# Kernel tuning notes

Measured on AMD Instinct MI355X. Metric: run time of the kernel, lower is better.

## Reference

```python
import jax, jax.numpy as jnp
import numpy as np

N_HEADS = 16
N_KV_HEADS = 8
DIM = 2048
HEAD_DIM = DIM // N_HEADS  # 128
N_REP = N_HEADS // N_KV_HEADS


def _rope(t, cos, sin):
    # t: [B, S, H, D]; cos/sin: [S, D//2]
    t2 = t.reshape(*t.shape[:-1], -1, 2)  # [B,S,H,D/2,2]
    p1, p2 = t2[..., 0], t2[..., 1]
    c = cos[None, :, None, :]
    s = sin[None, :, None, :]
    r1 = p1 * c - p2 * s
    r2 = p1 * s + p2 * c
    return jnp.stack((r1, r2), axis=-1).reshape(t.shape)


def setup_inputs() -> dict:
    key = jax.random.key(0)
    ks = jax.random.split(key, 7)
    B, S = 2, 2048
    x = jax.random.normal(ks[0], (B, S, DIM), dtype=jnp.float32)
    freqs_cos = jax.random.normal(ks[1], (S, HEAD_DIM // 2), dtype=jnp.float32)
    freqs_sin = jax.random.normal(ks[2], (S, HEAD_DIM // 2), dtype=jnp.float32)
    sc = 1.0 / np.sqrt(DIM)
    wq = jax.random.normal(ks[3], (DIM, N_HEADS * HEAD_DIM), dtype=jnp.float32) * sc
    wk = jax.random.normal(ks[4], (DIM, N_KV_HEADS * HEAD_DIM), dtype=jnp.float32) * sc
    wv = jax.random.normal(ks[5], (DIM, N_KV_HEADS * HEAD_DIM), dtype=jnp.float32) * sc
    wo = jax.random.normal(ks[6], (N_HEADS * HEAD_DIM, DIM), dtype=jnp.float32) * sc
    return {"x": x, "freqs_cos": freqs_cos, "freqs_sin": freqs_sin,
            "wq": wq, "wk": wk, "wv": wv, "wo": wo}


def reference(x, freqs_cos, freqs_sin, wq, wk, wv, wo):
    B, S, _ = x.shape
    xq = (x @ wq).reshape(B, S, N_HEADS, HEAD_DIM)
    xk = (x @ wk).reshape(B, S, N_KV_HEADS, HEAD_DIM)
    xv = (x @ wv).reshape(B, S, N_KV_HEADS, HEAD_DIM)
    xq = _rope(xq, freqs_cos, freqs_sin)
    xk = _rope(xk, freqs_cos, freqs_sin)
    # GQA repeat_kv: [B,S,Hkv,D] -> [B,S,Hkv*n_rep,D]
    xk = jnp.repeat(xk, N_REP, axis=2)
    xv = jnp.repeat(xv, N_REP, axis=2)
    q = xq.transpose(0, 2, 1, 3)  # [B,H,S,D]
    k = xk.transpose(0, 2, 1, 3)
    v = xv.transpose(0, 2, 1, 3)
    scale = 1.0 / np.sqrt(HEAD_DIM)
    scores = jnp.einsum('bhqd,bhkd->bhqk', q, k) * scale
    causal = jnp.tril(jnp.ones((S, S), dtype=bool))
    scores = jnp.where(causal[None, None], scores, -jnp.inf)
    probs = jax.nn.softmax(scores.astype(jnp.float32), axis=-1).astype(q.dtype)
    out = jnp.einsum('bhqk,bhkd->bhqd', probs, v)
    out = out.transpose(0, 2, 1, 3).reshape(B, S, N_HEADS * HEAD_DIM)
    return out @ wo
```

## Files before the change

### kernel.cpp

```cpp
#include <hip/hip_runtime.h>
#include <cstdint>
#include <cstddef>

#define S_LEN 2048
#define DIM_   2048
#define NH   16
#define NKV  8
#define HD   128

typedef __attribute__((ext_vector_type(8))) __bf16 bf16x8;
typedef __attribute__((ext_vector_type(4))) float  f32x4;

typedef const __attribute__((address_space(1))) void* gptr_t;
typedef __attribute__((address_space(3))) void*       sptr_t;

static __device__ __forceinline__ float bf2f(unsigned short u) {
  union { unsigned int i; float f; } v; v.i = ((unsigned int)u) << 16; return v.f;
}
static __device__ __forceinline__ unsigned short f2bf(float f) {
  union { float f; unsigned int i; } v; v.f = f;
  unsigned int u = v.i;
  unsigned int r = (u + 0x7FFFu + ((u >> 16) & 1u)) >> 16;
  return (unsigned short)r;
}

#define QSCALE 0.12751744f

__global__ void k_prep(const float* __restrict__ x, unsigned short* __restrict__ xb,
                       const float* __restrict__ wq, const float* __restrict__ wk,
                       const float* __restrict__ wv, const float* __restrict__ wo,
                       unsigned short* __restrict__ wqkvT, unsigned short* __restrict__ woT) {
  int bid = blockIdx.x;
  if (bid < 8192) {
    int i = bid * 256 + threadIdx.x;
    float4 v = ((const float4*)x)[i];
    ushort4 o; o.x = f2bf(v.x); o.y = f2bf(v.y); o.z = f2bf(v.z); o.w = f2bf(v.w);
    ((ushort4*)xb)[i] = o;
    return;
  }
  bid -= 8192;
  const float* src; unsigned short* dst; int N, ntx;
  if (bid < 4096)      { src = wq; dst = wqkvT;                       N = 2048; ntx = 64; }
  else if (bid < 6144) { bid -= 4096; src = wk; dst = wqkvT + (size_t)2048 * 2048; N = 1024; ntx = 32; }
  else if (bid < 8192) { bid -= 6144; src = wv; dst = wqkvT + (size_t)3072 * 2048; N = 1024; ntx = 32; }
  else                 { bid -= 8192; src = wo; dst = woT;            N = 2048; ntx = 64; }
  const int K = 2048;
  __shared__ float tile[32][33];
  int lx = threadIdx.x & 31, ly = threadIdx.x >> 5;
  int r0 = (bid / ntx) * 32, c0 = (bid % ntx) * 32;
  #pragma unroll
  for (int r = 0; r < 32; r += 8)
    tile[ly + r][lx] = src[(size_t)(r0 + ly + r) * N + c0 + lx];
  __syncthreads();
  #pragma unroll
  for (int r = 0; r < 32; r += 8)
    dst[(size_t)(c0 + ly + r) * K + r0 + lx] = f2bf(tile[lx][ly + r]);
}

template<int MODE>
__global__ __launch_bounds__(256, 2) void k_gemm_bt(
    const unsigned short* __restrict__ A, const unsigned short* __restrict__ BT,
    void* __restrict__ C, int N, int K,
    const float* __restrict__ fc, const float* __restrict__ fs,
    unsigned short* __restrict__ kb, unsigned short* __restrict__ vb) {
  __shared__ __align__(16) unsigned short Asm[128 * 64];
  __shared__ __align__(16) unsigned short Bsm[128 * 64];
  const int t = threadIdx.x;
  const int lane = t & 63, w = t >> 6;
  const int wm = (w >> 1) * 64, wn = (w & 1) * 64;
  const int col = lane & 15, quad = lane >> 4;
  const int m0 = blockIdx.y * 128, n0 = blockIdx.x * 128;

  f32x4 acc[4][4];
  #pragma unroll
  for (int i = 0; i < 4; i++)
    #pragma unroll
    for (int j = 0; j < 4; j++) acc[i][j] = (f32x4){0.f, 0.f, 0.f, 0.f};

  for (int kk = 0; kk < K; kk += 64) {
    #pragma unroll
    for (int r = 0; r < 4; ++r) {
      int c = t + r * 256;
      int c0 = (t & ~63) + r * 256;
      int row = c >> 3;
      int kcs = (c & 7) ^ (row & 7);
      const unsigned short* gA = A + (size_t)(m0 + row) * K + kk + kcs * 8;
      const unsigned short* gB = BT + (size_t)(n0 + row) * K + kk + kcs * 8;
      __builtin_amdgcn_global_load_lds((gptr_t)gA, (sptr_t)(&Asm[c0 * 8]), 16, 0, 0);
      __builtin_amdgcn_global_load_lds((gptr_t)gB, (sptr_t)(&Bsm[c0 * 8]), 16, 0, 0);
    }
    __syncthreads();
    #pragma unroll
    for (int kc2 = 0; kc2 < 2; kc2++) {
      bf16x8 af[4], bf[4];
      #pragma unroll
      for (int mi = 0; mi < 4; mi++) {
        int rowA = wm + mi * 16 + col;
        af[mi] = *(const bf16x8*)(&Asm[rowA * 64 + (((kc2 * 4 + quad) ^ (col & 7)) * 8)]);
      }
      #pragma unroll
      for (int ni = 0; ni < 4; ni++) {
        int rowB = wn + ni * 16 + col;
        bf[ni] = *(const bf16x8*)(&Bsm[rowB * 64 + (((kc2 * 4 + quad) ^ (col & 7)) * 8)]);
      }
      #pragma unroll
      for (int mi = 0; mi < 4; mi++)
        #pragma unroll
        for (int ni = 0; ni < 4; ni++)
          acc[mi][ni] = __builtin_amdgcn_mfma_f32_16x16x32_bf16(af[mi], bf[ni], acc[mi][ni], 0, 0, 0);
    }
    __syncthreads();
  }

  #pragma unroll
  for (int mi = 0; mi < 4; mi++) {
    int row_base = m0 + wm + mi * 16 + quad * 4;
    #pragma unroll
    for (int ni = 0; ni < 4; ni++) {
      int col_g = n0 + wn + ni * 16 + col;
      if (MODE == 1) {
        float* O = (float*)C;
        #pragma unroll
        for (int r = 0; r < 4; r++) O[(size_t)(row_base + r) * N + col_g] = acc[mi][ni][r];
      } else {
        int region = col_g >> 10;
        if (region < 3) {
          int ri = (col_g & 127) >> 1;
          float sgn = (col_g & 1) ? 1.f : -1.f;
          unsigned short* qO = (unsigned short*)C;
          #pragma unroll
          for (int r = 0; r < 4; r++) {
            int row = row_base + r;
            int s = row & (S_LEN - 1);
            float cv = fc[s * 64 + ri], sv = fs[s * 64 + ri];
            float val = acc[mi][ni][r];
            float other = __shfl_xor(val, 1);
            float res = val * cv + sgn * other * sv;
            if (region < 2) qO[(size_t)row * 2048 + col_g] = f2bf(res * QSCALE);
            else            kb[(size_t)row * 1024 + (col_g - 2048)] = f2bf(res);
          }
        } else {
          int n_local = col_g - 3072;
          int b = row_base >> 11, s = row_base & (S_LEN - 1);
          int kvh = n_local >> 7, d = n_local & (HD - 1);
          ushort4 o4;
          o4.x = f2bf(acc[mi][ni][0]); o4.y = f2bf(acc[mi][ni][1]);
          o4.z = f2bf(acc[mi][ni][2]); o4.w = f2bf(acc[mi][ni][3]);
          *(ushort4*)(&vb[((size_t)((b * NKV + kvh) * HD + d)) * S_LEN + s]) = o4;
        }
      }
    }
  }
}

#define KLD 136
#define VLD 72
__global__ __launch_bounds__(1024) void k_attn(
    const unsigned short* __restrict__ q, const unsigned short* __restrict__ k,
    const unsigned short* __restrict__ vT, unsigned short* __restrict__ ao) {
  __shared__ __align__(16) unsigned short Ksm[64 * KLD];
  __shared__ __align__(16) unsigned short Vsm[128 * VLD];
  __shared__ __align__(16) unsigned short Psm[16 * 16 * VLD];
  const int t = threadIdx.x;
  const int lane = t & 63, w = t >> 6;
  const int col = lane & 15, quad = lane >> 4;
  const int g = blockIdx.x;
  const int b = g >> 3, kvh = g & 7;
  const int h = kvh * 2 + ((w >> 2) & 1);
  const int y = blockIdx.y;
  const int my_qt = (w < 8) ? y : (31 - y);
  const int qrow = my_qt * 64 + (w & 3) * 16;
  unsigned short* Pw = &Psm[w * 16 * VLD];

  bf16x8 qf[4];
  const size_t qbase = ((size_t)(b * S_LEN) + qrow + col) * DIM_ + h * HD;
  #pragma unroll
  for (int kc = 0; kc < 4; kc++) qf[kc] = *(const bf16x8*)(q + qbase + kc * 32 + quad * 8);

  f32x4 o[8];
  #pragma unroll
  for (int i = 0; i < 8; i++) o[i] = (f32x4){0.f, 0.f, 0.f, 0.f};
  float m_i[4] = {-1e30f, -1e30f, -1e30f, -1e30f};
  float l_i[4] = {0.f, 0.f, 0.f, 0.f};

  const int nkt = 32 - y;
  for (int kt = 0; kt < nkt; ++kt) {
    { int i = t >> 4, dc = t & 15;
      *(uint4*)(&Ksm[i * KLD + dc * 8]) =
          *(const uint4*)(k + ((size_t)(b * S_LEN + kt * 64 + i)) * (NKV * HD) + kvh * HD + dc * 8);
      int d = t >> 3, kc2 = t & 7;
      *(uint4*)(&Vsm[d * VLD + kc2 * 8]) =
          *(const uint4*)(vT + ((size_t)((b * NKV + kvh) * HD + d)) * S_LEN + kt * 64 + kc2 * 8);
    }
    __syncthreads();

    if (kt <= my_qt) {
      float p[4][4];
      #pragma unroll
      for (int nt = 0; nt < 4; nt++) {
        f32x4 s_acc = (f32x4){0.f, 0.f, 0.f, 0.f};
        #pragma unroll
        for (int kc = 0; kc < 4; kc++) {
          bf16x8 kf = *(const bf16x8*)(&Ksm[(nt * 16 + col) * KLD + kc * 32 + quad * 8]);
          s_acc = __builtin_amdgcn_mfma_f32_16x16x32_bf16(qf[kc], kf, s_acc, 0, 0, 0);
        }
        #pragma unroll
        for (int r = 0; r < 4; r++) p[nt][r] = s_acc[r];
      }
      if (kt == my_qt) {
        #pragma unroll
        for (int nt = 0; nt < 4; nt++) {
          int key = kt * 64 + nt * 16 + col;
          #pragma unroll
          for (int r = 0; r < 4; r++) {
            int rg = qrow + quad * 4 + r;
            if (key > rg) p[nt][r] = -1e30f;
          }
        }
      }
      float mnew[4], alpha[4];
      #pragma unroll
      for (int r = 0; r < 4; r++) {
        float mx = fmaxf(fmaxf(p[0][r], p[1][r]), fmaxf(p[2][r], p[3][r]));
        mx = fmaxf(mx, __shfl_xor(mx, 1));
        mx = fmaxf(mx, __shfl_xor(mx, 2));
        mx = fmaxf(mx, __shfl_xor(mx, 4));
        mx = fmaxf(mx, __shfl_xor(mx, 8));
        mnew[r] = fmaxf(m_i[r], mx);
        alpha[r] = exp2f(m_i[r] - mnew[r]);
        m_i[r] = mnew[r];
      }
      float rsum[4] = {0.f, 0.f, 0.f, 0.f};
      #pragma unroll
      for (int nt = 0; nt < 4; nt++)
        #pragma unroll
        for (int r = 0; r < 4; r++) {
          float e = exp2f(p[nt][r] - mnew[r]);
          p[nt][r] = e;
          rsum[r] += e;
        }
      #pragma unroll
      for (int r = 0; r < 4; r++) {
        float rs = rsum[r];
        rs += __shfl_xor(rs, 1);
        rs += __shfl_xor(rs, 2);
        rs += __shfl_xor(rs, 4);
        rs += __shfl_xor(rs, 8);
        l_i[r] = l_i[r] * alpha[r] + rs;
      }
      #pragma unroll
      for (int dt = 0; dt < 8; dt++)
        #pragma unroll
        for (int r = 0; r < 4; r++) o[dt][r] *= alpha[r];

      #pragma unroll
      for (int nt = 0; nt < 4; nt++)
        #pragma unroll
        for (int r = 0; r < 4; r++)
          Pw[(quad * 4 + r) * VLD + nt * 16 + col] = f2bf(p[nt][r]);
      asm volatile("s_waitcnt lgkmcnt(0)" ::: "memory");
      bf16x8 pf[2];
      #pragma unroll
      for (int kc2 = 0; kc2 < 2; kc2++)
        pf[kc2] = *(const bf16x8*)(&Pw[col * VLD + kc2 * 32 + quad * 8]);

      #pragma unroll
      for (int dt = 0; dt < 8; dt++) {
        #pragma unroll
        for (int kc2 = 0; kc2 < 2; kc2++) {
          bf16x8 vf = *(const bf16x8*)(&Vsm[(dt * 16 + col) * VLD + kc2 * 32 + quad * 8]);
          o[dt] = __builtin_amdgcn_mfma_f32_16x16x32_bf16(pf[kc2], vf, o[dt], 0, 0, 0);
        }
      }
    }
    __syncthreads();
  }

  #pragma unroll
  for (int dt = 0; dt < 8; dt++) {
    int dcol = h * HD + dt * 16 + col;
    #pragma unroll
    for (int r = 0; r < 4; r++) {
      int rg = qrow + quad * 4 + r;
      ao[((size_t)(b * S_LEN) + rg) * DIM_ + dcol] = f2bf(o[dt][r] / l_i[r]);
    }
  }
}

extern "C" void kernel_launch(void* const* d_in, const int* in_sizes, int n_in,
                              void* d_out, int out_size, void* d_ws, size_t ws_size,
                              hipStream_t stream) {
  const float* x  = (const float*)d_in[0];
  const float* fc = (const float*)d_in[1];
  const float* fs = (const float*)d_in[2];
  const float* wq = (const float*)d_in[3];
  const float* wk = (const float*)d_in[4];
  const float* wv = (const float*)d_in[5];
  const float* wo = (const float*)d_in[6];
  float* out = (float*)d_out;

  char* ws = (char*)d_ws;
  const size_t MB = 1024 * 1024;
  unsigned short* xb    = (unsigned short*)(ws + 0 * MB);
  unsigned short* wqkvT = (unsigned short*)(ws + 16 * MB);
  unsigned short* woT   = (unsigned short*)(ws + 32 * MB);
  unsigned short* qb    = (unsigned short*)(ws + 40 * MB);
  unsigned short* kb    = (unsigned short*)(ws + 56 * MB);
  unsigned short* vT    = (unsigned short*)(ws + 64 * MB);
  unsigned short* ao    = (unsigned short*)(ws + 72 * MB);

  k_prep<<<dim3(20480), dim3(256), 0, stream>>>(x, xb, wq, wk, wv, wo, wqkvT, woT);
  k_gemm_bt<3><<<dim3(32, 32), dim3(256), 0, stream>>>(xb, wqkvT, (void*)qb, 4096, 2048, fc, fs, kb, vT);
  k_attn<<<dim3(16, 16), dim3(1024), 0, stream>>>(qb, kb, vT, ao);
  k_gemm_bt<1><<<dim3(16, 32), dim3(256), 0, stream>>>(ao, woT, (void*)out, 2048, 2048, nullptr, nullptr, nullptr, nullptr);
}
```

Measured before the change: 357.6 us.

## Transpose attention MFMA operands to keep P in registers and drop LDS staging

Swaps MFMA operand order so each lane holds a full query row's scores (query on the column index), so row max and sum need only two cross-quad shuffles and each lane keeps scalar m/l. The P tile is rebuilt for the PV MFMA by packing bf16 pairs and exchanging them through lane shuffles rather than a round trip through LDS, which also removes the Psm shared buffer. The output is now written as ushort4 vectors, and launch bounds add a min-blocks hint. The cost is many more shuffle instructions and selects per tile.

```diff
diff --git a/kernel.cpp b/kernel.cpp
--- a/kernel.cpp
+++ b/kernel.cpp
@@ -22,6 +22,9 @@
   unsigned int u = v.i;
   unsigned int r = (u + 0x7FFFu + ((u >> 16) & 1u)) >> 16;
   return (unsigned short)r;
+}
+static __device__ __forceinline__ unsigned int pack2bf(float lo, float hi) {
+  return ((unsigned int)f2bf(hi) << 16) | (unsigned int)f2bf(lo);
 }
 
 #define QSCALE 0.12751744f
@@ -155,12 +158,11 @@
 
 #define KLD 136
 #define VLD 72
-__global__ __launch_bounds__(1024) void k_attn(
+__global__ __launch_bounds__(1024, 4) void k_attn(
     const unsigned short* __restrict__ q, const unsigned short* __restrict__ k,
     const unsigned short* __restrict__ vT, unsigned short* __restrict__ ao) {
   __shared__ __align__(16) unsigned short Ksm[64 * KLD];
   __shared__ __align__(16) unsigned short Vsm[128 * VLD];
-  __shared__ __align__(16) unsigned short Psm[16 * 16 * VLD];
   const int t = threadIdx.x;
   const int lane = t & 63, w = t >> 6;
   const int col = lane & 15, quad = lane >> 4;
@@ -170,18 +172,21 @@
   const int y = blockIdx.y;
   const int my_qt = (w < 8) ? y : (31 - y);
   const int qrow = my_qt * 64 + (w & 3) * 16;
-  unsigned short* Pw = &Psm[w * 16 * VLD];
+  const int qg = qrow + col;
 
   bf16x8 qf[4];
-  const size_t qbase = ((size_t)(b * S_LEN) + qrow + col) * DIM_ + h * HD;
+  const size_t qbase = ((size_t)(b * S_LEN) + qg) * DIM_ + h * HD;
   #pragma unroll
   for (int kc = 0; kc < 4; kc++) qf[kc] = *(const bf16x8*)(q + qbase + kc * 32 + quad * 8);
 
   f32x4 o[8];
   #pragma unroll
   for (int i = 0; i < 8; i++) o[i] = (f32x4){0.f, 0.f, 0.f, 0.f};
-  float m_i[4] = {-1e30f, -1e30f, -1e30f, -1e30f};
-  float l_i[4] = {0.f, 0.f, 0.f, 0.f};
+  float m_i = -1e30f, l_i = 0.f;
+
+  const int ls0 = ((quad & 1) * 2) * 16 + col;
+  const int ls1 = ls0 + 16;
+  const bool hi_nt = (quad >> 1) != 0;
 
   const int nkt = 32 - y;
   for (int kt = 0; kt < nkt; ++kt) {
@@ -202,7 +207,7 @@
         #pragma unroll
         for (int kc = 0; kc < 4; kc++) {
           bf16x8 kf = *(const bf16x8*)(&Ksm[(nt * 16 + col) * KLD + kc * 32 + quad * 8]);
-          s_acc = __builtin_amdgcn_mfma_f32_16x16x32_bf16(qf[kc], kf, s_acc, 0, 0, 0);
+          s_acc = __builtin_amdgcn_mfma_f32_16x16x32_bf16(kf, qf[kc], s_acc, 0, 0, 0);
         }
         #pragma unroll
         for (int r = 0; r < 4; r++) p[nt][r] = s_acc[r];
@@ -210,80 +215,77 @@
       if (kt == my_qt) {
         #pragma unroll
         for (int nt = 0; nt < 4; nt++) {
-          int key = kt * 64 + nt * 16 + col;
+          int key = kt * 64 + nt * 16 + quad * 4;
           #pragma unroll
-          for (int r = 0; r < 4; r++) {
-            int rg = qrow + quad * 4 + r;
-            if (key > rg) p[nt][r] = -1e30f;
-          }
-        }
-      }
-      float mnew[4], alpha[4];
-      #pragma unroll
-      for (int r = 0; r < 4; r++) {
-        float mx = fmaxf(fmaxf(p[0][r], p[1][r]), fmaxf(p[2][r], p[3][r]));
-        mx = fmaxf(mx, __shfl_xor(mx, 1));
-        mx = fmaxf(mx, __shfl_xor(mx, 2));
-        mx = fmaxf(mx, __shfl_xor(mx, 4));
-        mx = fmaxf(mx, __shfl_xor(mx, 8));
-        mnew[r] = fmaxf(m_i[r], mx);
-        alpha[r] = exp2f(m_i[r] - mnew[r]);
-        m_i[r] = mnew[r];
-      }
-      float rsum[4] = {0.f, 0.f, 0.f, 0.f};
+          for (int r = 0; r < 4; r++)
+            if (key + r > qg) p[nt][r] = -1e30f;
+        }
+      }
+      float mx = p[0][0];
       #pragma unroll
       for (int nt = 0; nt < 4; nt++)
         #pragma unroll
+        for (int r = 0; r < 4; r++) mx = fmaxf(mx, p[nt][r]);
+      mx = fmaxf(mx, __shfl_xor(mx, 16));
+      mx = fmaxf(mx, __shfl_xor(mx, 32));
+      float mnew = fmaxf(m_i, mx);
+      float alpha = exp2f(m_i - mnew);
+      m_i = mnew;
+      float rs = 0.f;
+      #pragma unroll
+      for (int nt = 0; nt < 4; nt++)
+        #pragma unroll
         for (int r = 0; r < 4; r++) {
-          float e = exp2f(p[nt][r] - mnew[r]);
+          float e = exp2f(p[nt][r] - mnew);
           p[nt][r] = e;
-          rsum[r] += e;
-        }
-      #pragma unroll
-      for (int r = 0; r < 4; r++) {
-        float rs = rsum[r];
-        rs += __shfl_xor(rs, 1);
-        rs += __shfl_xor(rs, 2);
-        rs += __shfl_xor(rs, 4);
-        rs += __shfl_xor(rs, 8);
-        l_i[r] = l_i[r] * alpha[r] + rs;
-      }
+          rs += e;
+        }
+      rs += __shfl_xor(rs, 16);
+      rs += __shfl_xor(rs, 32);
+      l_i = l_i * alpha + rs;
       #pragma unroll
       for (int dt = 0; dt < 8; dt++)
         #pragma unroll
-        for (int r = 0; r < 4; r++) o[dt][r] *= alpha[r];
-
-      #pragma unroll
-      for (int nt = 0; nt < 4; nt++)
-        #pragma unroll
-        for (int r = 0; r < 4; r++)
-          Pw[(quad * 4 + r) * VLD + nt * 16 + col] = f2bf(p[nt][r]);
-      asm volatile("s_waitcnt lgkmcnt(0)" ::: "memory");
-      bf16x8 pf[2];
-      #pragma unroll
-      for (int kc2 = 0; kc2 < 2; kc2++)
-        pf[kc2] = *(const bf16x8*)(&Pw[col * VLD + kc2 * 32 + quad * 8]);
-
-      #pragma unroll
-      for (int dt = 0; dt < 8; dt++) {
-        #pragma unroll
-        for (int kc2 = 0; kc2 < 2; kc2++) {
+        for (int r = 0; r < 4; r++) o[dt][r] *= alpha;
+
+      unsigned int pk[4][2];
+      #pragma unroll
+      for (int nt = 0; nt < 4; nt++) {
+        pk[nt][0] = pack2bf(p[nt][0], p[nt][1]);
+        pk[nt][1] = pack2bf(p[nt][2], p[nt][3]);
+      }
+      #pragma unroll
+      for (int kc2 = 0; kc2 < 2; kc2++) {
+        union { bf16x8 v; unsigned int d[4]; } pf;
+        unsigned int a0 = (unsigned int)__shfl((int)pk[2 * kc2][0], ls0);
+        unsigned int b0 = (unsigned int)__shfl((int)pk[2 * kc2 + 1][0], ls0);
+        pf.d[0] = hi_nt ? b0 : a0;
+        unsigned int a1 = (unsigned int)__shfl((int)pk[2 * kc2][1], ls0);
+        unsigned int b1 = (unsigned int)__shfl((int)pk[2 * kc2 + 1][1], ls0);
+        pf.d[1] = hi_nt ? b1 : a1;
+        unsigned int a2 = (unsigned int)__shfl((int)pk[2 * kc2][0], ls1);
+        unsigned int b2 = (unsigned int)__shfl((int)pk[2 * kc2 + 1][0], ls1);
+        pf.d[2] = hi_nt ? b2 : a2;
+        unsigned int a3 = (unsigned int)__shfl((int)pk[2 * kc2][1], ls1);
+        unsigned int b3 = (unsigned int)__shfl((int)pk[2 * kc2 + 1][1], ls1);
+        pf.d[3] = hi_nt ? b3 : a3;
+        #pragma unroll
+        for (int dt = 0; dt < 8; dt++) {
           bf16x8 vf = *(const bf16x8*)(&Vsm[(dt * 16 + col) * VLD + kc2 * 32 + quad * 8]);
-          o[dt] = __builtin_amdgcn_mfma_f32_16x16x32_bf16(pf[kc2], vf, o[dt], 0, 0, 0);
+          o[dt] = __builtin_amdgcn_mfma_f32_16x16x32_bf16(vf, pf.v, o[dt], 0, 0, 0);
         }
       }
     }
     __syncthreads();
   }
 
+  float inv = 1.f / l_i;
   #pragma unroll
   for (int dt = 0; dt < 8; dt++) {
-    int dcol = h * HD + dt * 16 + col;
-    #pragma unroll
-    for (int r = 0; r < 4; r++) {
-      int rg = qrow + quad * 4 + r;
-      ao[((size_t)(b * S_LEN) + rg) * DIM_ + dcol] = f2bf(o[dt][r] / l_i[r]);
-    }
+    ushort4 o4;
+    o4.x = f2bf(o[dt][0] * inv); o4.y = f2bf(o[dt][1] * inv);
+    o4.z = f2bf(o[dt][2] * inv); o4.w = f2bf(o[dt][3] * inv);
+    *(ushort4*)(&ao[((size_t)(b * S_LEN) + qg) * DIM_ + h * HD + dt * 16 + quad * 4]) = o4;
   }
 }
 
```

After: 359.2 us. Within noise of the previous version (+0.4%).
